# Optimization experiments

Measured on AMD Instinct MI355X. Metric: run time of the kernel, lower is better.

## Reference

```python
import jax, jax.numpy as jnp
import numpy as np
from jax import lax

SIGMA = 0.8
THRESH_MIN = 50.0
THRESH_MAX = 80.0
TRACK_CONN = 5
TRACK_ITERS = 3


def _gaussian_kernel(sigma=SIGMA):
    ks = int(((sigma - 0.8) / 0.3 + 1) * 2 + 1)
    ks += 1 if ks % 2 == 0 else 0
    ax = np.arange(-ks // 2 + 1.0, ks // 2 + 1.0)
    xx, yy = np.meshgrid(ax, ax)
    normal = 1 / (2.0 * np.pi * sigma ** 2)
    k = np.exp(-(xx ** 2 + yy ** 2) / (2.0 * sigma ** 2)) * normal
    k = k / np.sum(k)
    return k.reshape(ks, ks, 1, 1).astype(np.float32)


def _sobel_kernel():
    gx = np.array([[-1, 0, 1], [-2, 0, 2], [-1, 0, 1]], dtype=np.float32)
    gy = np.array([[1, 2, 1], [0, 0, 0], [-1, -2, -1]], dtype=np.float32)
    return np.stack([gx, gy], axis=-1).reshape(3, 3, 1, 2)


def setup_inputs() -> dict:
    key = jax.random.key(0)
    x = jax.random.uniform(key, (8, 1024, 1024, 1), dtype=jnp.float32) * 255.0
    return {
        'x': x,
        'gaussian_kernel': jnp.asarray(_gaussian_kernel()),
        'sobel_kernel': jnp.asarray(_sobel_kernel()),
    }


def _conv_same(x, k):
    return lax.conv_general_dilated(x, k, (1, 1), 'SAME',
                                    dimension_numbers=('NHWC', 'HWIO', 'NHWC'))


# offsets with kernel value 0 (others are -inf) for the 4 angle NMS kernels
_ANGLE_OFFSETS = [
    [(0, -1), (0, 0), (0, 1)],     # 0 deg
    [(-1, 1), (0, 0), (1, -1)],    # 45 deg
    [(-1, 0), (0, 0), (1, 0)],     # 90 deg
    [(-1, -1), (0, 0), (1, 1)],    # 135 deg
]


def _angle_dilation(ar):
    # morphological dilation (tf.nn.dilation2d) with -inf masked 3x3 kernels,
    # realized as max over the 3 unmasked shifts per angle channel.
    B, H, W, _ = ar.shape
    pad = jnp.pad(ar, ((0, 0), (1, 1), (1, 1), (0, 0)),
                  constant_values=-jnp.inf)
    outs = []
    for c, offs in enumerate(_ANGLE_OFFSETS):
        ch = pad[..., c]
        m = ch[:, 1 + offs[0][0]:1 + offs[0][0] + H, 1 + offs[0][1]:1 + offs[0][1] + W]
        for dy, dx in offs[1:]:
            m = jnp.maximum(m, ch[:, 1 + dy:1 + dy + H, 1 + dx:1 + dx + W])
        outs.append(m)
    return jnp.stack(outs, axis=-1)


def _canny(x, gaussian_kernel, sobel_kernel):
    dt = x.dtype
    x_smooth = _conv_same(x, gaussian_kernel)
    grad_xy = _conv_same(x_smooth, sobel_kernel)
    gx, gy = grad_xy[..., 0:1], grad_xy[..., 1:2]
    theta = (jnp.arctan2(gy, gx) * (180.0 / np.pi) + 90.0) % 180.0
    grad_mag = jnp.clip(jnp.sqrt(gx * gx + gy * gy), 0.0, 255.0)

    # angle-bucketed masks (channels: 0, 45, 90, 135 deg)
    m0 = (theta >= 157.5) | (theta <= 22.5)
    m1 = (theta >= 22.5) & (theta < 67.5)
    m2 = (theta >= 67.5) & (theta < 112.5)
    m3 = (theta >= 112.5) & (theta < 157.5)
    masks = jnp.concatenate([m0, m1, m2, m3], axis=-1).astype(dt)
    angle_responses = masks * grad_mag  # (B,H,W,4)

    max_pool_angle = _angle_dilation(angle_responses)

    # non-max suppression + double threshold
    suppressed = jnp.where(max_pool_angle == angle_responses, grad_mag, 0.0)
    edge_candidates = jnp.max(suppressed, axis=-1, keepdims=True)
    strong = (edge_candidates >= THRESH_MAX).astype(dt)
    weak = ((edge_candidates >= THRESH_MIN) & (edge_candidates < THRESH_MAX)).astype(dt)

    # iterative hysteresis: weak pixels adjacent (within KxK window) to strong
    # pixels become strong
    win = (1, TRACK_CONN, TRACK_CONN, 1)
    for _ in range(TRACK_ITERS):
        pooled = lax.reduce_window(strong, -jnp.inf, lax.max, win,
                                   (1, 1, 1, 1), 'SAME')
        strong = jnp.clip(strong + weak * pooled, 0.0, 1.0)
    return strong.astype(dt)


def reference(x, gaussian_kernel, sobel_kernel):
    return _canny(x, gaussian_kernel, sobel_kernel)
```

## Files before the change

### kernel.cpp

```cpp
#include <hip/hip_runtime.h>
#include <math.h>

#define NT   512
#define TS   64
#define HX   9
#define XR   82
#define XSTR 84
#define ST   80
#define SSTR 82
#define MT   78
#define DSTR 39
#define WT   76
#define WPR  3
#define HB   6

#define POOLA ((XR*XSTR*4 + 15) & ~15)

template<bool IN>
__device__ __forceinline__ void canny_tile(
    const float* __restrict__ xb, const float* __restrict__ g,
    float* __restrict__ ob, int H, int W, int ty0, int tx0, int tid,
    float* __restrict__ s_x, float* __restrict__ s_mag,
    unsigned char* __restrict__ s_dirn, float* __restrict__ s_sm,
    unsigned char* __restrict__ s_byte, unsigned int* __restrict__ s_bs,
    unsigned int* __restrict__ s_bw, unsigned int* __restrict__ s_bh)
{
  for (int i = tid; i < XR*XSTR; i += NT) {
    int r = i / XSTR, c = i - r*XSTR;
    int gy = ty0 + r - HX, gx = tx0 + c - HX;
    float v = 0.f;
    if (IN || ((unsigned)gy < (unsigned)H && (unsigned)gx < (unsigned)W))
      v = xb[(size_t)gy*W + gx];
    s_x[i] = v;
  }
  __syncthreads();

  for (int i = tid; i < ST*(ST/2); i += NT) {
    int r = i / (ST/2), pc = i - r*(ST/2);
    int c0 = 2*pc;
    const float* xr = &s_x[r*XSTR + c0];
    float2 q00 = *(const float2*)(xr),        q01 = *(const float2*)(xr+2);
    float2 q10 = *(const float2*)(xr+XSTR),   q11 = *(const float2*)(xr+XSTR+2);
    float2 q20 = *(const float2*)(xr+2*XSTR), q21 = *(const float2*)(xr+2*XSTR+2);
    int gy  = ty0 + r - (HX-1);
    int gx0 = tx0 + c0 - (HX-1);
    float a0 = 0.f, a1 = 0.f;
    if (IN || ((unsigned)gy < (unsigned)H && (unsigned)gx0 < (unsigned)W)) {
      float acc = 0.f;
      acc += q00.x*g[0]; acc += q00.y*g[1]; acc += q01.x*g[2];
      acc += q10.x*g[3]; acc += q10.y*g[4]; acc += q11.x*g[5];
      acc += q20.x*g[6]; acc += q20.y*g[7]; acc += q21.x*g[8];
      a0 = acc;
    }
    if (IN || ((unsigned)gy < (unsigned)H && (unsigned)(gx0+1) < (unsigned)W)) {
      float acc = 0.f;
      acc += q00.y*g[0]; acc += q01.x*g[1]; acc += q01.y*g[2];
      acc += q10.y*g[3]; acc += q11.x*g[4]; acc += q11.y*g[5];
      acc += q20.y*g[6]; acc += q21.x*g[7]; acc += q21.y*g[8];
      a1 = acc;
    }
    *(float2*)&s_sm[r*SSTR + c0] = make_float2(a0, a1);
  }
  __syncthreads();

  for (int i = tid; i < MT*(MT/2); i += NT) {
    int r = i / (MT/2), pc = i - r*(MT/2);
    int c0 = 2*pc;
    const float* sm0 = &s_sm[r*SSTR + c0];
    float2 p00=*(const float2*)(sm0),         p01=*(const float2*)(sm0+2);
    float2 p10=*(const float2*)(sm0+SSTR),    p11=*(const float2*)(sm0+SSTR+2);
    float2 p20=*(const float2*)(sm0+2*SSTR),  p21=*(const float2*)(sm0+2*SSTR+2);
    float v00=p00.x, v01=p00.y, v02=p01.x, v03=p01.y;
    float v10=p10.x, v11=p10.y, v12=p11.x, v13=p11.y;
    float v20=p20.x, v21=p20.y, v22=p21.x, v23=p21.y;
    unsigned int dpair = 0;
    float m0v = 0.f, m1v = 0.f;
    int gy  = ty0 + r - (HX-2);
    int gxb = tx0 + c0 - (HX-2);
#pragma unroll
    for (int half = 0; half < 2; ++half) {
      float a00 = half ? v01 : v00, a01 = half ? v02 : v01, a02 = half ? v03 : v02;
      float a10 = half ? v11 : v10,                          a12 = half ? v13 : v12;
      float a20 = half ? v21 : v20, a21 = half ? v22 : v21, a22 = half ? v23 : v22;
      float mag = 0.f; unsigned int dir = 0;
      if (IN || ((unsigned)gy < (unsigned)H && (unsigned)(gxb+half) < (unsigned)W)) {
        float fgx = 0.f - a00;
        fgx += a02;
        fgx = fmaf(a10, -2.f, fgx);
        fgx = fmaf(a12,  2.f, fgx);
        fgx -= a20;
        fgx += a22;
        float fgy = a00;
        fgy = fmaf(a01, 2.f, fgy);
        fgy += a02;
        fgy -= a20;
        fgy = fmaf(a21, -2.f, fgy);
        fgy -= a22;
        mag = fminf(sqrtf(fgx*fgx + fgy*fgy), 255.f);
        float ax = fabsf(fgx), ay = fabsf(fgy);
        float sum = ax + ay;
        float d1 = ay - 0.41421356237f*ax;
        float d2 = ay - 2.41421356237f*ax;
        float band = 1e-4f * sum;
        if (sum == 0.f) {
          dir = 4;
        } else if (fabsf(d1) >= band && fabsf(d2) >= band) {
          if (d2 > 0.f)      dir = 1;
          else if (d1 < 0.f) dir = 4;
          else dir = (((__float_as_uint(fgx) ^ __float_as_uint(fgy)) >> 31) & 1)
                       ? 2 : 8;
        } else {
          float th = atan2f(fgy, fgx) * 57.29577951308232f + 90.0f;
          if (th < 0.f) th += 180.f; else if (th >= 180.f) th -= 180.f;
          if (th >= 157.5f || th <= 22.5f)  dir |= 1;
          if (th >= 22.5f  && th < 67.5f)   dir |= 2;
          if (th >= 67.5f  && th < 112.5f)  dir |= 4;
          if (th >= 112.5f && th < 157.5f)  dir |= 8;
        }
      }
      if (half == 0) m0v = mag; else m1v = mag;
      dpair |= dir << (4*half);
    }
    *(float2*)&s_mag[r*MT + c0] = make_float2(m0v, m1v);
    s_dirn[r*DSTR + pc] = (unsigned char)dpair;
  }
  __syncthreads();

  for (int i = tid; i < WT*(WT/2); i += NT) {
    int r = i / (WT/2), j = i - r*(WT/2);
    int cb = 2*j;
    const float* mrow = &s_mag[r*MT + cb];
    float2 t0a = *(const float2*)(mrow),        t0b = *(const float2*)(mrow+2);
    float2 t1a = *(const float2*)(mrow+MT),     t1b = *(const float2*)(mrow+MT+2);
    float2 t2a = *(const float2*)(mrow+2*MT),   t2b = *(const float2*)(mrow+2*MT+2);
    const unsigned char* drow = &s_dirn[r*DSTR + j];
    unsigned int d0 = drow[0]        | ((unsigned int)drow[1] << 8);
    unsigned int d1 = drow[DSTR]     | ((unsigned int)drow[DSTR+1] << 8);
    unsigned int d2 = drow[2*DSTR]   | ((unsigned int)drow[2*DSTR+1] << 8);
    float m0[4] = {t0a.x, t0a.y, t0b.x, t0b.y};
    float m1[4] = {t1a.x, t1a.y, t1b.x, t1b.y};
    float m2[4] = {t2a.x, t2a.y, t2b.x, t2b.y};
    unsigned int out2 = 0;
#pragma unroll
    for (int k = 0; k < 2; ++k) {
      float mag = m1[k+1];
      unsigned int dc = (d1 >> (4*(k+1))) & 0xFu;
      bool keep = false;
      {
        float rp = (dc & 1) ? mag : 0.f;
        float a  = ((d1 >> (4*k))     & 1) ? m1[k]   : 0.f;
        float bb = ((d1 >> (4*(k+2))) & 1) ? m1[k+2] : 0.f;
        keep = keep || (a <= rp && bb <= rp);
      }
      {
        float rp = (dc & 2) ? mag : 0.f;
        float a  = ((d0 >> (4*(k+2))) & 2) ? m0[k+2] : 0.f;
        float bb = ((d2 >> (4*k))     & 2) ? m2[k]   : 0.f;
        keep = keep || (a <= rp && bb <= rp);
      }
      {
        float rp = (dc & 4) ? mag : 0.f;
        float a  = ((d0 >> (4*(k+1))) & 4) ? m0[k+1] : 0.f;
        float bb = ((d2 >> (4*(k+1))) & 4) ? m2[k+1] : 0.f;
        keep = keep || (a <= rp && bb <= rp);
      }
      {
        float rp = (dc & 8) ? mag : 0.f;
        float a  = ((d0 >> (4*k))     & 8) ? m0[k]   : 0.f;
        float bb = ((d2 >> (4*(k+2))) & 8) ? m2[k+2] : 0.f;
        keep = keep || (a <= rp && bb <= rp);
      }
      unsigned int v = keep ? ((mag >= 80.f) ? 2u : ((mag >= 50.f) ? 1u : 0u)) : 0u;
      out2 |= v << (8*k);
    }
    *(unsigned short*)&s_byte[r*WT + cb] = (unsigned short)out2;
  }
  __syncthreads();

  for (int i = tid; i < WT*WPR; i += NT) {
    int r = i / WPR, k = i - r*WPR;
    const unsigned char* row = &s_byte[r*WT + 32*k];
    int nw = (k < 2) ? 8 : 3;
    unsigned int sb = 0, wb = 0;
#pragma unroll
    for (int q = 0; q < 8; ++q) {
      if (q < nw) {
        unsigned int w = *(const unsigned int*)(row + 4*q);
        unsigned int t = (w >> 1) & 0x01010101u;
        unsigned int u = w & 0x01010101u;
        sb |= (((t * 0x01020408u) >> 24) & 0xFu) << (4*q);
        wb |= (((u * 0x01020408u) >> 24) & 0xFu) << (4*q);
      }
    }
    s_bs[r*WPR + k] = sb;
    s_bw[r*WPR + k] = wb;
  }
  __syncthreads();

#pragma unroll
  for (int it = 0; it < 3; ++it) {
    for (int i = tid; i < WT*WPR; i += NT) {
      int r = i / WPR, k = i - r*WPR;
      unsigned int s  = s_bs[r*WPR + k];
      unsigned int lo = (k > 0)     ? s_bs[r*WPR + k - 1] : 0u;
      unsigned int hi = (k < WPR-1) ? s_bs[r*WPR + k + 1] : 0u;
      s_bh[r*WPR + k] = s | (s<<1) | (s<<2) | (s>>1) | (s>>2)
                          | (lo>>30) | (lo>>31) | (hi<<30) | (hi<<31);
    }
    __syncthreads();
    for (int i = tid; i < (WT-4)*WPR; i += NT) {
      int r = i / WPR + 2, k = i - (r-2)*WPR;
      unsigned int p = s_bh[(r-2)*WPR + k] | s_bh[(r-1)*WPR + k] | s_bh[r*WPR + k]
                     | s_bh[(r+1)*WPR + k] | s_bh[(r+2)*WPR + k];
      s_bs[r*WPR + k] |= (s_bw[r*WPR + k] & p);
    }
    __syncthreads();
  }

  if (IN) {
    for (int i = tid; i < TS*(TS/4); i += NT) {
      int r = i >> 4, mq = i & 15;
      int cc0 = 4*mq + HB;
      int rr = r + HB;
      int k0 = cc0 >> 5;
      unsigned long long wp = (unsigned long long)s_bs[rr*WPR + k0]
                            | ((unsigned long long)s_bs[rr*WPR + k0 + 1] << 32);
      unsigned int bits = (unsigned int)(wp >> (cc0 & 31));
      float4 o;
      o.x = (float)(bits & 1u);
      o.y = (float)((bits >> 1) & 1u);
      o.z = (float)((bits >> 2) & 1u);
      o.w = (float)((bits >> 3) & 1u);
      *(float4*)&ob[(size_t)(ty0+r)*W + tx0 + 4*mq] = o;
    }
  } else {
    for (int i = tid; i < TS*TS; i += NT) {
      int r = i / TS, c = i - r*TS;
      int oy = ty0 + r, ox = tx0 + c;
      if (oy < H && ox < W) {
        int rr = r + HB, cc = c + HB;
        unsigned int w = s_bs[rr*WPR + (cc >> 5)];
        ob[(size_t)oy*W + ox] = (float)((w >> (cc & 31)) & 1u);
      }
    }
  }
}

__global__ __launch_bounds__(NT) void canny_fused(
    const float* __restrict__ x, const float* __restrict__ gk,
    float* __restrict__ out, int H, int W, int tilesX, int tilesY)
{
  __shared__ __align__(16) unsigned char poolA[POOLA];
  float* s_x   = (float*)poolA;
  float* s_mag = (float*)poolA;
  unsigned char* s_dirn = poolA + MT*MT*4;
  __shared__ __align__(16) float s_sm[ST*SSTR];
  unsigned char* s_byte = (unsigned char*)s_sm;
  unsigned int* s_bs = (unsigned int*)((unsigned char*)s_sm + 5776);
  unsigned int* s_bw = s_bs + WT*WPR;
  unsigned int* s_bh = s_bw + WT*WPR;

  const int tpi = tilesX * tilesY;
  const int b  = blockIdx.x / tpi;
  const int t  = blockIdx.x % tpi;
  const int ty0 = (t / tilesX) * TS;
  const int tx0 = (t % tilesX) * TS;
  const float* xb = x + (size_t)b * H * W;
  float* ob = out + (size_t)b * H * W;
  const int tid = threadIdx.x;

  float g[9];
#pragma unroll
  for (int i = 0; i < 9; ++i) g[i] = gk[i];

  const bool interior = (ty0 >= HX) && (ty0 + XR - HX <= H)
                     && (tx0 >= HX) && (tx0 + XSTR - HX < W);
  if (interior)
    canny_tile<true >(xb, g, ob, H, W, ty0, tx0, tid,
                      s_x, s_mag, s_dirn, s_sm, s_byte, s_bs, s_bw, s_bh);
  else
    canny_tile<false>(xb, g, ob, H, W, ty0, tx0, tid,
                      s_x, s_mag, s_dirn, s_sm, s_byte, s_bs, s_bw, s_bh);
}

extern "C" void kernel_launch(void* const* d_in, const int* in_sizes, int n_in,
                              void* d_out, int out_size, void* d_ws, size_t ws_size,
                              hipStream_t stream)
{
  const float* x  = (const float*)d_in[0];
  const float* gk = (const float*)d_in[1];
  float* out = (float*)d_out;

  const int H = 1024, W = 1024;
  const int B = in_sizes[0] / (H * W);
  const int tilesX = (W + TS - 1) / TS, tilesY = (H + TS - 1) / TS;

  dim3 grid(B * tilesX * tilesY);
  canny_fused<<<grid, NT, 0, stream>>>(x, gk, out, H, W, tilesX, tilesY);
}
```

Baseline: 146.6 us.

## Use 1024-thread blocks with 2x4 register micro-tiles and fused hysteresis passes

Doubles the block to 1024 threads and gives each thread a 2x4 output micro-tile in the Gaussian, Sobel and NMS stages, loading a 4x6 register window with float4 loads so neighbours are reused instead of reloaded. The hysteresis loop is merged into one pass per iteration using ping-pong bitmask buffers, which halves the barriers there. Shared-memory strides and layouts change (direction stored as one byte per pixel, padded rows), and the interior test becomes slightly looser. Larger blocks may lower occupancy and raise register pressure, and many threads sit idle in stages that have fewer work items than threads.

```diff
diff --git a/kernel.cpp b/kernel.cpp
--- a/kernel.cpp
+++ b/kernel.cpp
@@ -1,29 +1,29 @@
 #include <hip/hip_runtime.h>
 #include <math.h>
 
-#define NT   512
+#define NT   1024
 #define TS   64
 #define HX   9
 #define XR   82
 #define XSTR 84
 #define ST   80
-#define SSTR 82
+#define SSTR 84
 #define MT   78
-#define DSTR 39
+#define MSTR 80
 #define WT   76
 #define WPR  3
 #define HB   6
 
-#define POOLA ((XR*XSTR*4 + 15) & ~15)
+#define POOLA 31200
 
 template<bool IN>
 __device__ __forceinline__ void canny_tile(
     const float* __restrict__ xb, const float* __restrict__ g,
     float* __restrict__ ob, int H, int W, int ty0, int tx0, int tid,
     float* __restrict__ s_x, float* __restrict__ s_mag,
-    unsigned char* __restrict__ s_dirn, float* __restrict__ s_sm,
-    unsigned char* __restrict__ s_byte, unsigned int* __restrict__ s_bs,
-    unsigned int* __restrict__ s_bw, unsigned int* __restrict__ s_bh)
+    unsigned char* __restrict__ s_dirb, float* __restrict__ s_sm,
+    unsigned char* __restrict__ s_byte, unsigned int* __restrict__ s_bsA,
+    unsigned int* __restrict__ s_bsB, unsigned int* __restrict__ s_bw)
 {
   for (int i = tid; i < XR*XSTR; i += NT) {
     int r = i / XSTR, c = i - r*XSTR;
@@ -35,150 +35,166 @@
   }
   __syncthreads();
 
-  for (int i = tid; i < ST*(ST/2); i += NT) {
-    int r = i / (ST/2), pc = i - r*(ST/2);
-    int c0 = 2*pc;
-    const float* xr = &s_x[r*XSTR + c0];
-    float2 q00 = *(const float2*)(xr),        q01 = *(const float2*)(xr+2);
-    float2 q10 = *(const float2*)(xr+XSTR),   q11 = *(const float2*)(xr+XSTR+2);
-    float2 q20 = *(const float2*)(xr+2*XSTR), q21 = *(const float2*)(xr+2*XSTR+2);
-    int gy  = ty0 + r - (HX-1);
-    int gx0 = tx0 + c0 - (HX-1);
-    float a0 = 0.f, a1 = 0.f;
-    if (IN || ((unsigned)gy < (unsigned)H && (unsigned)gx0 < (unsigned)W)) {
-      float acc = 0.f;
-      acc += q00.x*g[0]; acc += q00.y*g[1]; acc += q01.x*g[2];
-      acc += q10.x*g[3]; acc += q10.y*g[4]; acc += q11.x*g[5];
-      acc += q20.x*g[6]; acc += q20.y*g[7]; acc += q21.x*g[8];
-      a0 = acc;
-    }
-    if (IN || ((unsigned)gy < (unsigned)H && (unsigned)(gx0+1) < (unsigned)W)) {
-      float acc = 0.f;
-      acc += q00.y*g[0]; acc += q01.x*g[1]; acc += q01.y*g[2];
-      acc += q10.y*g[3]; acc += q11.x*g[4]; acc += q11.y*g[5];
-      acc += q20.y*g[6]; acc += q21.x*g[7]; acc += q21.y*g[8];
-      a1 = acc;
-    }
-    *(float2*)&s_sm[r*SSTR + c0] = make_float2(a0, a1);
-  }
-  __syncthreads();
-
-  for (int i = tid; i < MT*(MT/2); i += NT) {
-    int r = i / (MT/2), pc = i - r*(MT/2);
-    int c0 = 2*pc;
-    const float* sm0 = &s_sm[r*SSTR + c0];
-    float2 p00=*(const float2*)(sm0),         p01=*(const float2*)(sm0+2);
-    float2 p10=*(const float2*)(sm0+SSTR),    p11=*(const float2*)(sm0+SSTR+2);
-    float2 p20=*(const float2*)(sm0+2*SSTR),  p21=*(const float2*)(sm0+2*SSTR+2);
-    float v00=p00.x, v01=p00.y, v02=p01.x, v03=p01.y;
-    float v10=p10.x, v11=p10.y, v12=p11.x, v13=p11.y;
-    float v20=p20.x, v21=p20.y, v22=p21.x, v23=p21.y;
-    unsigned int dpair = 0;
-    float m0v = 0.f, m1v = 0.f;
-    int gy  = ty0 + r - (HX-2);
-    int gxb = tx0 + c0 - (HX-2);
-#pragma unroll
-    for (int half = 0; half < 2; ++half) {
-      float a00 = half ? v01 : v00, a01 = half ? v02 : v01, a02 = half ? v03 : v02;
-      float a10 = half ? v11 : v10,                          a12 = half ? v13 : v12;
-      float a20 = half ? v21 : v20, a21 = half ? v22 : v21, a22 = half ? v23 : v22;
-      float mag = 0.f; unsigned int dir = 0;
-      if (IN || ((unsigned)gy < (unsigned)H && (unsigned)(gxb+half) < (unsigned)W)) {
-        float fgx = 0.f - a00;
-        fgx += a02;
-        fgx = fmaf(a10, -2.f, fgx);
-        fgx = fmaf(a12,  2.f, fgx);
-        fgx -= a20;
-        fgx += a22;
-        float fgy = a00;
-        fgy = fmaf(a01, 2.f, fgy);
-        fgy += a02;
-        fgy -= a20;
-        fgy = fmaf(a21, -2.f, fgy);
-        fgy -= a22;
-        mag = fminf(sqrtf(fgx*fgx + fgy*fgy), 255.f);
-        float ax = fabsf(fgx), ay = fabsf(fgy);
-        float sum = ax + ay;
-        float d1 = ay - 0.41421356237f*ax;
-        float d2 = ay - 2.41421356237f*ax;
-        float band = 1e-4f * sum;
-        if (sum == 0.f) {
-          dir = 4;
-        } else if (fabsf(d1) >= band && fabsf(d2) >= band) {
-          if (d2 > 0.f)      dir = 1;
-          else if (d1 < 0.f) dir = 4;
-          else dir = (((__float_as_uint(fgx) ^ __float_as_uint(fgy)) >> 31) & 1)
-                       ? 2 : 8;
-        } else {
-          float th = atan2f(fgy, fgx) * 57.29577951308232f + 90.0f;
-          if (th < 0.f) th += 180.f; else if (th >= 180.f) th -= 180.f;
-          if (th >= 157.5f || th <= 22.5f)  dir |= 1;
-          if (th >= 22.5f  && th < 67.5f)   dir |= 2;
-          if (th >= 67.5f  && th < 112.5f)  dir |= 4;
-          if (th >= 112.5f && th < 157.5f)  dir |= 8;
-        }
-      }
-      if (half == 0) m0v = mag; else m1v = mag;
-      dpair |= dir << (4*half);
-    }
-    *(float2*)&s_mag[r*MT + c0] = make_float2(m0v, m1v);
-    s_dirn[r*DSTR + pc] = (unsigned char)dpair;
-  }
-  __syncthreads();
-
-  for (int i = tid; i < WT*(WT/2); i += NT) {
-    int r = i / (WT/2), j = i - r*(WT/2);
-    int cb = 2*j;
-    const float* mrow = &s_mag[r*MT + cb];
-    float2 t0a = *(const float2*)(mrow),        t0b = *(const float2*)(mrow+2);
-    float2 t1a = *(const float2*)(mrow+MT),     t1b = *(const float2*)(mrow+MT+2);
-    float2 t2a = *(const float2*)(mrow+2*MT),   t2b = *(const float2*)(mrow+2*MT+2);
-    const unsigned char* drow = &s_dirn[r*DSTR + j];
-    unsigned int d0 = drow[0]        | ((unsigned int)drow[1] << 8);
-    unsigned int d1 = drow[DSTR]     | ((unsigned int)drow[DSTR+1] << 8);
-    unsigned int d2 = drow[2*DSTR]   | ((unsigned int)drow[2*DSTR+1] << 8);
-    float m0[4] = {t0a.x, t0a.y, t0b.x, t0b.y};
-    float m1[4] = {t1a.x, t1a.y, t1b.x, t1b.y};
-    float m2[4] = {t2a.x, t2a.y, t2b.x, t2b.y};
-    unsigned int out2 = 0;
-#pragma unroll
-    for (int k = 0; k < 2; ++k) {
-      float mag = m1[k+1];
-      unsigned int dc = (d1 >> (4*(k+1))) & 0xFu;
-      bool keep = false;
-      {
-        float rp = (dc & 1) ? mag : 0.f;
-        float a  = ((d1 >> (4*k))     & 1) ? m1[k]   : 0.f;
-        float bb = ((d1 >> (4*(k+2))) & 1) ? m1[k+2] : 0.f;
-        keep = keep || (a <= rp && bb <= rp);
-      }
-      {
-        float rp = (dc & 2) ? mag : 0.f;
-        float a  = ((d0 >> (4*(k+2))) & 2) ? m0[k+2] : 0.f;
-        float bb = ((d2 >> (4*k))     & 2) ? m2[k]   : 0.f;
-        keep = keep || (a <= rp && bb <= rp);
-      }
-      {
-        float rp = (dc & 4) ? mag : 0.f;
-        float a  = ((d0 >> (4*(k+1))) & 4) ? m0[k+1] : 0.f;
-        float bb = ((d2 >> (4*(k+1))) & 4) ? m2[k+1] : 0.f;
-        keep = keep || (a <= rp && bb <= rp);
-      }
-      {
-        float rp = (dc & 8) ? mag : 0.f;
-        float a  = ((d0 >> (4*k))     & 8) ? m0[k]   : 0.f;
-        float bb = ((d2 >> (4*(k+2))) & 8) ? m2[k+2] : 0.f;
-        keep = keep || (a <= rp && bb <= rp);
-      }
-      unsigned int v = keep ? ((mag >= 80.f) ? 2u : ((mag >= 50.f) ? 1u : 0u)) : 0u;
-      out2 |= v << (8*k);
-    }
-    *(unsigned short*)&s_byte[r*WT + cb] = (unsigned short)out2;
-  }
-  __syncthreads();
-
-  for (int i = tid; i < WT*WPR; i += NT) {
-    int r = i / WPR, k = i - r*WPR;
+  if (tid < 800) {
+    int qr = tid / 20, qc = tid - qr*20;
+    int r0 = 2*qr, c0 = 4*qc;
+    float xq[4][6];
+#pragma unroll
+    for (int j = 0; j < 4; ++j) {
+      const float* xr = &s_x[(r0+j)*XSTR + c0];
+      float4 a = *(const float4*)xr;
+      float2 bq = *(const float2*)(xr+4);
+      xq[j][0]=a.x; xq[j][1]=a.y; xq[j][2]=a.z; xq[j][3]=a.w;
+      xq[j][4]=bq.x; xq[j][5]=bq.y;
+    }
+#pragma unroll
+    for (int ry = 0; ry < 2; ++ry) {
+      float o[4];
+#pragma unroll
+      for (int k = 0; k < 4; ++k) {
+        int gy = ty0 + (r0+ry) - (HX-1), gx = tx0 + (c0+k) - (HX-1);
+        float acc = 0.f;
+        if (IN || ((unsigned)gy < (unsigned)H && (unsigned)gx < (unsigned)W)) {
+#pragma unroll
+          for (int dy = 0; dy < 3; ++dy)
+#pragma unroll
+            for (int dx = 0; dx < 3; ++dx)
+              acc += xq[ry+dy][k+dx] * g[dy*3+dx];
+        }
+        o[k] = acc;
+      }
+      *(float4*)&s_sm[(r0+ry)*SSTR + c0] = make_float4(o[0],o[1],o[2],o[3]);
+    }
+  } else if (tid < 880) {
+    int r = tid - 800;
+    *(float4*)&s_sm[r*SSTR + ST] = make_float4(0.f,0.f,0.f,0.f);
+  }
+  __syncthreads();
+
+  if (tid < 780) {
+    int qr = tid / 20, qc = tid - qr*20;
+    int r0 = 2*qr, c0 = 4*qc;
+    float sq[4][6];
+#pragma unroll
+    for (int j = 0; j < 4; ++j) {
+      const float* sr = &s_sm[(r0+j)*SSTR + c0];
+      float4 a = *(const float4*)sr;
+      float2 bq = *(const float2*)(sr+4);
+      sq[j][0]=a.x; sq[j][1]=a.y; sq[j][2]=a.z; sq[j][3]=a.w;
+      sq[j][4]=bq.x; sq[j][5]=bq.y;
+    }
+#pragma unroll
+    for (int ry = 0; ry < 2; ++ry) {
+      float mg[4]; unsigned int dw = 0;
+#pragma unroll
+      for (int k = 0; k < 4; ++k) {
+        float a00=sq[ry][k],   a01=sq[ry][k+1],   a02=sq[ry][k+2];
+        float a10=sq[ry+1][k],                    a12=sq[ry+1][k+2];
+        float a20=sq[ry+2][k], a21=sq[ry+2][k+1], a22=sq[ry+2][k+2];
+        float mag = 0.f; unsigned int dir = 0;
+        int gy = ty0 + (r0+ry) - (HX-2), gx = tx0 + (c0+k) - (HX-2);
+        if (IN || ((unsigned)gy < (unsigned)H && (unsigned)gx < (unsigned)W)) {
+          float fgx = 0.f - a00;
+          fgx += a02;
+          fgx = fmaf(a10, -2.f, fgx);
+          fgx = fmaf(a12,  2.f, fgx);
+          fgx -= a20;
+          fgx += a22;
+          float fgy = a00;
+          fgy = fmaf(a01, 2.f, fgy);
+          fgy += a02;
+          fgy -= a20;
+          fgy = fmaf(a21, -2.f, fgy);
+          fgy -= a22;
+          mag = fminf(sqrtf(fgx*fgx + fgy*fgy), 255.f);
+          float ax = fabsf(fgx), ay = fabsf(fgy);
+          float sum = ax + ay;
+          float d1 = ay - 0.41421356237f*ax;
+          float d2 = ay - 2.41421356237f*ax;
+          float band = 1e-4f * sum;
+          if (sum == 0.f) {
+            dir = 4;
+          } else if (fabsf(d1) >= band && fabsf(d2) >= band) {
+            if (d2 > 0.f)      dir = 1;
+            else if (d1 < 0.f) dir = 4;
+            else dir = (((__float_as_uint(fgx) ^ __float_as_uint(fgy)) >> 31) & 1)
+                         ? 2 : 8;
+          } else {
+            float th = atan2f(fgy, fgx) * 57.29577951308232f + 90.0f;
+            if (th < 0.f) th += 180.f; else if (th >= 180.f) th -= 180.f;
+            if (th >= 157.5f || th <= 22.5f)  dir |= 1;
+            if (th >= 22.5f  && th < 67.5f)   dir |= 2;
+            if (th >= 67.5f  && th < 112.5f)  dir |= 4;
+            if (th >= 112.5f && th < 157.5f)  dir |= 8;
+          }
+        }
+        mg[k] = mag;
+        dw |= dir << (8*k);
+      }
+      *(float4*)&s_mag[(r0+ry)*MSTR + c0] = make_float4(mg[0],mg[1],mg[2],mg[3]);
+      *(unsigned int*)&s_dirb[(r0+ry)*MSTR + c0] = dw;
+    }
+  }
+  __syncthreads();
+
+  if (tid < 722) {
+    int qr = tid / 19, qc = tid - qr*19;
+    int r0 = 2*qr, c0 = 4*qc;
+    float mq[4][6]; unsigned long long dq[4];
+#pragma unroll
+    for (int j = 0; j < 4; ++j) {
+      const float* mr = &s_mag[(r0+j)*MSTR + c0];
+      float4 a = *(const float4*)mr;
+      float2 bq = *(const float2*)(mr+4);
+      mq[j][0]=a.x; mq[j][1]=a.y; mq[j][2]=a.z; mq[j][3]=a.w;
+      mq[j][4]=bq.x; mq[j][5]=bq.y;
+      const unsigned char* dr = &s_dirb[(r0+j)*MSTR + c0];
+      dq[j] = (unsigned long long)(*(const unsigned int*)dr)
+            | ((unsigned long long)(*(const unsigned short*)(dr+4)) << 32);
+    }
+#pragma unroll
+    for (int ry = 0; ry < 2; ++ry) {
+      unsigned int outw = 0;
+      unsigned long long d0 = dq[ry], d1 = dq[ry+1], d2 = dq[ry+2];
+#pragma unroll
+      for (int k = 0; k < 4; ++k) {
+        float mag = mq[ry+1][k+1];
+        unsigned int dc = (unsigned int)(d1 >> (8*(k+1))) & 0xFu;
+        bool keep = false;
+        {
+          float rp = (dc & 1) ? mag : 0.f;
+          float a  = ((d1 >> (8*k))     & 1) ? mq[ry+1][k]   : 0.f;
+          float bb = ((d1 >> (8*(k+2))) & 1) ? mq[ry+1][k+2] : 0.f;
+          keep = keep || (a <= rp && bb <= rp);
+        }
+        {
+          float rp = (dc & 2) ? mag : 0.f;
+          float a  = ((d0 >> (8*(k+2))) & 2) ? mq[ry][k+2]   : 0.f;
+          float bb = ((d2 >> (8*k))     & 2) ? mq[ry+2][k]   : 0.f;
+          keep = keep || (a <= rp && bb <= rp);
+        }
+        {
+          float rp = (dc & 4) ? mag : 0.f;
+          float a  = ((d0 >> (8*(k+1))) & 4) ? mq[ry][k+1]   : 0.f;
+          float bb = ((d2 >> (8*(k+1))) & 4) ? mq[ry+2][k+1] : 0.f;
+          keep = keep || (a <= rp && bb <= rp);
+        }
+        {
+          float rp = (dc & 8) ? mag : 0.f;
+          float a  = ((d0 >> (8*k))     & 8) ? mq[ry][k]     : 0.f;
+          float bb = ((d2 >> (8*(k+2))) & 8) ? mq[ry+2][k+2] : 0.f;
+          keep = keep || (a <= rp && bb <= rp);
+        }
+        unsigned int v = keep ? ((mag >= 80.f) ? 2u : ((mag >= 50.f) ? 1u : 0u)) : 0u;
+        outw |= v << (8*k);
+      }
+      *(unsigned int*)&s_byte[(r0+ry)*WT + c0] = outw;
+    }
+  }
+  __syncthreads();
+
+  if (tid < WT*WPR) {
+    int r = tid / WPR, k = tid - r*WPR;
     const unsigned char* row = &s_byte[r*WT + 32*k];
     int nw = (k < 2) ? 8 : 3;
     unsigned int sb = 0, wb = 0;
@@ -192,73 +208,74 @@
         wb |= (((u * 0x01020408u) >> 24) & 0xFu) << (4*q);
       }
     }
-    s_bs[r*WPR + k] = sb;
-    s_bw[r*WPR + k] = wb;
+    s_bsA[tid] = sb;
+    s_bsB[tid] = sb;
+    s_bw[tid]  = wb;
   }
   __syncthreads();
 
 #pragma unroll
   for (int it = 0; it < 3; ++it) {
-    for (int i = tid; i < WT*WPR; i += NT) {
-      int r = i / WPR, k = i - r*WPR;
-      unsigned int s  = s_bs[r*WPR + k];
-      unsigned int lo = (k > 0)     ? s_bs[r*WPR + k - 1] : 0u;
-      unsigned int hi = (k < WPR-1) ? s_bs[r*WPR + k + 1] : 0u;
-      s_bh[r*WPR + k] = s | (s<<1) | (s<<2) | (s>>1) | (s>>2)
-                          | (lo>>30) | (lo>>31) | (hi<<30) | (hi<<31);
+    const unsigned int* src = (it == 1) ? s_bsB : s_bsA;
+    unsigned int*       dst = (it == 1) ? s_bsA : s_bsB;
+    if (tid < (WT-4)*WPR) {
+      int r = tid / WPR + 2, k = tid - (r-2)*WPR;
+      unsigned int p = 0, selfw = 0;
+#pragma unroll
+      for (int dr = 0; dr < 5; ++dr) {
+        int row = r - 2 + dr;
+        unsigned int s  = src[row*WPR + k];
+        unsigned int lo = (k > 0)     ? src[row*WPR + k - 1] : 0u;
+        unsigned int hi = (k < WPR-1) ? src[row*WPR + k + 1] : 0u;
+        p |= s | (s<<1) | (s<<2) | (s>>1) | (s>>2)
+               | (lo>>30) | (lo>>31) | (hi<<30) | (hi<<31);
+        if (dr == 2) selfw = s;
+      }
+      dst[r*WPR + k] = selfw | (s_bw[r*WPR + k] & p);
     }
     __syncthreads();
-    for (int i = tid; i < (WT-4)*WPR; i += NT) {
-      int r = i / WPR + 2, k = i - (r-2)*WPR;
-      unsigned int p = s_bh[(r-2)*WPR + k] | s_bh[(r-1)*WPR + k] | s_bh[r*WPR + k]
-                     | s_bh[(r+1)*WPR + k] | s_bh[(r+2)*WPR + k];
-      s_bs[r*WPR + k] |= (s_bw[r*WPR + k] & p);
-    }
-    __syncthreads();
   }
 
   if (IN) {
-    for (int i = tid; i < TS*(TS/4); i += NT) {
-      int r = i >> 4, mq = i & 15;
-      int cc0 = 4*mq + HB;
-      int rr = r + HB;
-      int k0 = cc0 >> 5;
-      unsigned long long wp = (unsigned long long)s_bs[rr*WPR + k0]
-                            | ((unsigned long long)s_bs[rr*WPR + k0 + 1] << 32);
-      unsigned int bits = (unsigned int)(wp >> (cc0 & 31));
-      float4 o;
-      o.x = (float)(bits & 1u);
-      o.y = (float)((bits >> 1) & 1u);
-      o.z = (float)((bits >> 2) & 1u);
-      o.w = (float)((bits >> 3) & 1u);
-      *(float4*)&ob[(size_t)(ty0+r)*W + tx0 + 4*mq] = o;
-    }
+    int r = tid >> 4, mq = tid & 15;
+    int cc0 = 4*mq + HB;
+    int rr = r + HB;
+    int k0 = cc0 >> 5;
+    unsigned long long wp = (unsigned long long)s_bsB[rr*WPR + k0]
+                          | ((unsigned long long)s_bsB[rr*WPR + k0 + 1] << 32);
+    unsigned int bits = (unsigned int)(wp >> (cc0 & 31));
+    float4 o;
+    o.x = (float)(bits & 1u);
+    o.y = (float)((bits >> 1) & 1u);
+    o.z = (float)((bits >> 2) & 1u);
+    o.w = (float)((bits >> 3) & 1u);
+    *(float4*)&ob[(size_t)(ty0+r)*W + tx0 + 4*mq] = o;
   } else {
     for (int i = tid; i < TS*TS; i += NT) {
       int r = i / TS, c = i - r*TS;
       int oy = ty0 + r, ox = tx0 + c;
       if (oy < H && ox < W) {
         int rr = r + HB, cc = c + HB;
-        unsigned int w = s_bs[rr*WPR + (cc >> 5)];
+        unsigned int w = s_bsB[rr*WPR + (cc >> 5)];
         ob[(size_t)oy*W + ox] = (float)((w >> (cc & 31)) & 1u);
       }
     }
   }
 }
 
-__global__ __launch_bounds__(NT) void canny_fused(
+__global__ __launch_bounds__(NT, 8) void canny_fused(
     const float* __restrict__ x, const float* __restrict__ gk,
     float* __restrict__ out, int H, int W, int tilesX, int tilesY)
 {
   __shared__ __align__(16) unsigned char poolA[POOLA];
   float* s_x   = (float*)poolA;
   float* s_mag = (float*)poolA;
-  unsigned char* s_dirn = poolA + MT*MT*4;
+  unsigned char* s_dirb = poolA + MT*MSTR*4;
   __shared__ __align__(16) float s_sm[ST*SSTR];
   unsigned char* s_byte = (unsigned char*)s_sm;
-  unsigned int* s_bs = (unsigned int*)((unsigned char*)s_sm + 5776);
-  unsigned int* s_bw = s_bs + WT*WPR;
-  unsigned int* s_bh = s_bw + WT*WPR;
+  unsigned int* s_bsA = (unsigned int*)((unsigned char*)s_sm + 5792);
+  unsigned int* s_bsB = s_bsA + WT*WPR;
+  unsigned int* s_bw  = s_bsB + WT*WPR;
 
   const int tpi = tilesX * tilesY;
   const int b  = blockIdx.x / tpi;
@@ -274,13 +291,13 @@
   for (int i = 0; i < 9; ++i) g[i] = gk[i];
 
   const bool interior = (ty0 >= HX) && (ty0 + XR - HX <= H)
-                     && (tx0 >= HX) && (tx0 + XSTR - HX < W);
+                     && (tx0 >= HX) && (tx0 + XSTR - HX <= W);
   if (interior)
     canny_tile<true >(xb, g, ob, H, W, ty0, tx0, tid,
-                      s_x, s_mag, s_dirn, s_sm, s_byte, s_bs, s_bw, s_bh);
+                      s_x, s_mag, s_dirb, s_sm, s_byte, s_bsA, s_bsB, s_bw);
   else
     canny_tile<false>(xb, g, ob, H, W, ty0, tx0, tid,
-                      s_x, s_mag, s_dirn, s_sm, s_byte, s_bs, s_bw, s_bh);
+                      s_x, s_mag, s_dirb, s_sm, s_byte, s_bsA, s_bsB, s_bw);
 }
 
 extern "C" void kernel_launch(void* const* d_in, const int* in_sizes, int n_in,
```

After: 140.1 us. 1.05x faster.
